# Kernel tuning notes

Hardware: AMD Instinct MI355X
Metric: run time of the kernel (lower is better)

## Reference

```python
import jax, jax.numpy as jnp
import numpy as np

HID = 256      # hidden_dim
EXPAND = 2
D_INNER = HID * EXPAND
LN_EPS = 1e-5


def _gru(xs, W_ih, W_hh, b_ih, b_hh):
    """torch nn.GRU (batch_first) over axis 1. xs: (N, P, d_inner) -> (N, P, H).
    Gate order (torch): r, z, n."""
    N = xs.shape[0]
    Hd = W_hh.shape[0]
    gi = xs @ W_ih + b_ih                 # (N, P, 3H) - input gates precomputed
    gi = jnp.swapaxes(gi, 0, 1)           # (P, N, 3H) for scan over P
    h0 = jnp.zeros((N, Hd), xs.dtype)

    def step(h, gi_t):
        gh = h @ W_hh + b_hh              # (N, 3H)
        ir, iz, i_n = jnp.split(gi_t, 3, axis=-1)
        hr, hz, h_n = jnp.split(gh, 3, axis=-1)
        r = jax.nn.sigmoid(ir + hr)
        z = jax.nn.sigmoid(iz + hz)
        n = jnp.tanh(i_n + r * h_n)
        h = (1.0 - z) * n + z * h
        return h, h

    _, ys = jax.lax.scan(step, h0, gi)    # (P, N, H)
    return jnp.swapaxes(ys, 0, 1)


def _branch(x2d, lin_W, lin_b, W_ih, W_hh, b_ih, b_hh):
    # Linear -> exact GELU (torch nn.GELU default) -> GRU
    h = jax.nn.gelu(x2d @ lin_W + lin_b, approximate=False)
    return _gru(h, W_ih, W_hh, b_ih, b_hh)


def setup_inputs() -> dict:
    key = jax.random.key(0)
    ks = jax.random.split(key, 16)
    s = 0.05
    p = {
        "x": jax.random.normal(ks[0], (8, 16, 1024, HID), jnp.float32),
        "fwd_lin_W": jax.random.normal(ks[1], (HID, D_INNER)) * s,
        "fwd_lin_b": jnp.zeros((D_INNER,)),
        "fwd_W_ih": jax.random.normal(ks[2], (D_INNER, 3 * HID)) * s,
        "fwd_W_hh": jax.random.normal(ks[3], (HID, 3 * HID)) * s,
        "fwd_b_ih": jnp.zeros((3 * HID,)),
        "fwd_b_hh": jnp.zeros((3 * HID,)),
        "bwd_lin_W": jax.random.normal(ks[4], (HID, D_INNER)) * s,
        "bwd_lin_b": jnp.zeros((D_INNER,)),
        "bwd_W_ih": jax.random.normal(ks[5], (D_INNER, 3 * HID)) * s,
        "bwd_W_hh": jax.random.normal(ks[6], (HID, 3 * HID)) * s,
        "bwd_b_ih": jnp.zeros((3 * HID,)),
        "bwd_b_hh": jnp.zeros((3 * HID,)),
        "proj_W": jax.random.normal(ks[7], (2 * HID, HID)) * s,
        "proj_b": jnp.zeros((HID,)),
        "ln_g": jnp.ones((HID,)),
        "ln_b": jnp.zeros((HID,)),
    }
    return p


def reference(x, fwd_lin_W, fwd_lin_b, fwd_W_ih, fwd_W_hh, fwd_b_ih, fwd_b_hh,
              bwd_lin_W, bwd_lin_b, bwd_W_ih, bwd_W_hh, bwd_b_ih, bwd_b_hh,
              proj_W, proj_b, ln_g, ln_b):
    B, T, P, H = x.shape
    xf = x.reshape(B * T, P, H)  # every timestep gets the identical spatial pass
    f_out = _branch(xf, fwd_lin_W, fwd_lin_b, fwd_W_ih, fwd_W_hh, fwd_b_ih, fwd_b_hh)
    b_out = _branch(xf[:, ::-1], bwd_lin_W, bwd_lin_b, bwd_W_ih, bwd_W_hh, bwd_b_ih, bwd_b_hh)[:, ::-1]
    cat = jnp.concatenate([f_out, b_out], axis=-1)          # (BT, P, 2H)
    out = cat @ proj_W + proj_b                              # (BT, P, H)
    out = out.reshape(B, T, P, H) + x                        # residual
    mu = out.mean(-1, keepdims=True)
    var = out.var(-1, keepdims=True)
    return (out - mu) * jax.lax.rsqrt(var + LN_EPS) * ln_g + ln_b
```

## Files before the change

kernel.cpp:

```cpp
#include <hip/hip_runtime.h>
#include <cmath>


typedef _Float16 h8  __attribute__((ext_vector_type(8)));
typedef _Float16 h2v __attribute__((ext_vector_type(2)));
typedef float    f32x4 __attribute__((ext_vector_type(4)));

#define MTOT 131072L
#define PSEQ 1024

__device__ __forceinline__ float fast_sigmoid(float x) {
    float e = __builtin_amdgcn_exp2f(-1.44269504089f * x);
    return __builtin_amdgcn_rcpf(1.f + e);
}
__device__ __forceinline__ float fast_tanh(float x) {
    float e = __builtin_amdgcn_exp2f(-2.88539008178f * x);
    return (1.f - e) * __builtin_amdgcn_rcpf(1.f + e);
}

template <int MODE>
__global__ __launch_bounds__(256) void k_gemm(
    const void* __restrict__ Aa_, const void* __restrict__ Ab_,
    const float* __restrict__ B, const float* __restrict__ bias,
    const float* __restrict__ xres, void* __restrict__ out_, long m_off)
{
    constexpr int K = (MODE == 0) ? 256 : 512;
    constexpr int N = (MODE == 0) ? 512 : (MODE == 1 ? 768 : 256);

    __shared__ __align__(16) _Float16 Al[64][40];
    __shared__ __align__(16) _Float16 Bl[64][40];

    const int tid  = threadIdx.x;
    const int lane = tid & 63;
    const int wave = tid >> 6;
    const int wm = wave >> 1, wn = wave & 1;
    const long bm0 = (long)(MODE == 1 ? blockIdx.y : blockIdx.x) * 64;
    const int  bn0 = (MODE == 1 ? blockIdx.x : blockIdx.y) * 64;

    const int sm  = tid >> 2;
    const int ska = (tid & 3) * 8;
    const int sn  = tid & 63;
    const int skb = (tid >> 6) * 8;

    f32x4 acc[2][2] = {};

    for (int kt = 0; kt < K / 32; ++kt) {
        h8 av;
        if constexpr (MODE == 0) {
            const float* ap = (const float*)Aa_ + (bm0 + sm) * 256 + kt * 32 + ska;
            #pragma unroll
            for (int i = 0; i < 8; ++i) av[i] = (_Float16)ap[i];
        } else if constexpr (MODE == 1) {
            av = *(const h8*)((const _Float16*)Aa_ + (bm0 + sm) * 512 + kt * 32 + ska);
        } else {
            const _Float16* src = (kt < 8) ? (const _Float16*)Aa_ : (const _Float16*)Ab_;
            av = *(const h8*)(src + (bm0 + sm) * 256 + (kt & 7) * 32 + ska);
        }
        *(h8*)&Al[sm][ska] = av;

        h8 bv;
        #pragma unroll
        for (int i = 0; i < 8; ++i)
            bv[i] = (_Float16)B[(long)(kt * 32 + skb + i) * N + bn0 + sn];
        *(h8*)&Bl[sn][skb] = bv;

        __syncthreads();

        const int fr = lane & 15, fg = lane >> 4;
        h8 a0 = *(const h8*)&Al[wm * 32 +      fr][fg * 8];
        h8 a1 = *(const h8*)&Al[wm * 32 + 16 + fr][fg * 8];
        h8 b0 = *(const h8*)&Bl[wn * 32 +      fr][fg * 8];
        h8 b1 = *(const h8*)&Bl[wn * 32 + 16 + fr][fg * 8];
        acc[0][0] = __builtin_amdgcn_mfma_f32_16x16x32_f16(a0, b0, acc[0][0], 0, 0, 0);
        acc[0][1] = __builtin_amdgcn_mfma_f32_16x16x32_f16(a0, b1, acc[0][1], 0, 0, 0);
        acc[1][0] = __builtin_amdgcn_mfma_f32_16x16x32_f16(a1, b0, acc[1][0], 0, 0, 0);
        acc[1][1] = __builtin_amdgcn_mfma_f32_16x16x32_f16(a1, b1, acc[1][1], 0, 0, 0);

        __syncthreads();
    }

    const int fr = lane & 15, fg = lane >> 4;
    #pragma unroll
    for (int fm = 0; fm < 2; ++fm)
    #pragma unroll
    for (int fn = 0; fn < 2; ++fn)
    #pragma unroll
    for (int r = 0; r < 4; ++r) {
        long row = bm0 + wm * 32 + fm * 16 + fg * 4 + r;
        int  col = bn0 + wn * 32 + fn * 16 + fr;
        float v = acc[fm][fn][r] + bias[col];
        if constexpr (MODE == 0) {
            v = 0.5f * v * (1.0f + erff(v * 0.70710678118654752f));
            ((_Float16*)out_)[row * (long)N + col] = (_Float16)v;
        } else if constexpr (MODE == 1) {
            long grow = row + m_off;
            int seq = (int)(grow >> 10), p = (int)(grow & 1023);
            int blk = seq >> 4, srow = seq & 15;
            int g = col >> 8, ci = col & 255;
            int wv = ci >> 5, tp = (ci >> 4) & 1;
            int ln = (ci & 15) | ((srow >> 2) << 4);
            int e = tp * 4 + (srow & 3);
            long oidx = (((long)(blk * 1024 + p) * 3 + g) * 512 + (wv * 64 + ln)) * 8 + e;
            ((_Float16*)out_)[oidx] = (_Float16)v;
        } else {
            v += xres[row * 256 + col];
            ((float*)out_)[row * 256 + col] = v;
        }
    }
}

__global__ __launch_bounds__(256) void k_prep_frag(
    const float* __restrict__ Whh, _Float16* __restrict__ Wp)
{
    const int t = blockIdx.x * 256 + threadIdx.x;
    const int l = t & 63, f = t >> 6;
    const int kt = f & 7;
    const int q  = f >> 3;
    const int tp = q & 1;
    const int q2 = q >> 1;
    const int g  = q2 % 3, w = q2 / 3;
    const int col = g * 256 + w * 32 + tp * 16 + (l & 15);
    const int k0  = kt * 32 + (l >> 4) * 8;
    h8 v;
    #pragma unroll
    for (int i = 0; i < 8; ++i)
        v[i] = (_Float16)Whh[(long)(k0 + i) * 768 + col];
    ((h8*)Wp)[t] = v;
}

__global__ __launch_bounds__(256) void k_prep_bias(
    const float* __restrict__ bih, const float* __restrict__ bhh, float* __restrict__ bc)
{
    const int c = blockIdx.x * 256 + threadIdx.x;
    bc[c] = bih[c] + (c < 512 ? bhh[c] : 0.f);
}

__global__ __launch_bounds__(512, 2) void k_gru2(
    const _Float16* __restrict__ gpf, const _Float16* __restrict__ gpb,
    const _Float16* __restrict__ Wpf, const _Float16* __restrict__ Wpb,
    const float* __restrict__ bhhf, const float* __restrict__ bhhb,
    _Float16* __restrict__ hof, _Float16* __restrict__ hob)
{
    const int b = blockIdx.x;
    const int dir = b & 1;
    const int blk = b >> 1;
    const int t = threadIdx.x;
    const int w = t >> 6, l = t & 63;
    const int lr = l & 15, lq = l >> 4;

    const _Float16* gp  = dir ? gpb : gpf;
    const _Float16* Wp  = dir ? Wpb : Wpf;
    const float*    bhh = dir ? bhhb : bhhf;
    _Float16*       hoo = dir ? hob : hof;

    __shared__ __align__(16) h8 wn_lds[8192];
    __shared__ __align__(16) _Float16 hbuf[2][16][264];

    h8 bfrz[2][2][8];
    {
        const h8* src = (const h8*)Wp + (long)w * 48 * 64 + l;
        #pragma unroll
        for (int g = 0; g < 2; ++g)
        #pragma unroll
        for (int tp = 0; tp < 2; ++tp)
        #pragma unroll
        for (int kt = 0; kt < 8; ++kt)
            bfrz[g][tp][kt] = src[((g * 2 + tp) * 8 + kt) * 64];
        #pragma unroll
        for (int tp = 0; tp < 2; ++tp)
        #pragma unroll
        for (int kt = 0; kt < 8; ++kt)
            wn_lds[((w * 2 + tp) * 8 + kt) * 64 + l] = src[((4 + tp) * 8 + kt) * 64];
    }
    const int col0 = w * 32 + lr;
    const float bn0 = bhh[512 + col0];
    const float bn1 = bhh[512 + col0 + 16];

    for (int i = t; i < 2 * 16 * 264; i += 512) ((_Float16*)hbuf)[i] = (_Float16)0.f;
    __syncthreads();

    const int d = dir ? -1 : 1;
    int p = dir ? (PSEQ - 1) : 0;
    int cur = 0;
    const long tbase = (long)t * 8;
    const long bbase = (long)blk * 1024;
    float hold[2][4] = {};

    h8 gv0 = *(const h8*)(gp + ((bbase + p) * 3 + 0) * 4096 + tbase);
    h8 gv1 = *(const h8*)(gp + ((bbase + p) * 3 + 1) * 4096 + tbase);
    h8 gv2 = *(const h8*)(gp + ((bbase + p) * 3 + 2) * 4096 + tbase);

    for (int step = 0; step < PSEQ; ++step) {
        int pn = p + d;
        pn = pn < 0 ? 0 : (pn > PSEQ - 1 ? PSEQ - 1 : pn);
        h8 nv0 = *(const h8*)(gp + ((bbase + pn) * 3 + 0) * 4096 + tbase);
        h8 nv1 = *(const h8*)(gp + ((bbase + pn) * 3 + 1) * 4096 + tbase);
        h8 nv2 = *(const h8*)(gp + ((bbase + pn) * 3 + 2) * 4096 + tbase);

        h8 af[8];
        #pragma unroll
        for (int kt = 0; kt < 8; ++kt)
            af[kt] = *(const h8*)&hbuf[cur][lr][kt * 32 + lq * 8];

        f32x4 accr[2] = {}, accz[2] = {};
        #pragma unroll
        for (int kt = 0; kt < 8; ++kt) {
            #pragma unroll
            for (int tp = 0; tp < 2; ++tp) {
                accr[tp] = __builtin_amdgcn_mfma_f32_16x16x32_f16(af[kt], bfrz[0][tp][kt], accr[tp], 0, 0, 0);
                accz[tp] = __builtin_amdgcn_mfma_f32_16x16x32_f16(af[kt], bfrz[1][tp][kt], accz[tp], 0, 0, 0);
            }
        }

        float rr[2][4], zz[2][4];
        #pragma unroll
        for (int tp = 0; tp < 2; ++tp)
        #pragma unroll
        for (int r = 0; r < 4; ++r) {
            const int e = tp * 4 + r;
            rr[tp][r] = fast_sigmoid(accr[tp][r] + (float)gv0[e]);
            zz[tp][r] = fast_sigmoid(accz[tp][r] + (float)gv1[e]);
        }

        f32x4 accn[2] = {};
        #pragma unroll
        for (int kt = 0; kt < 8; ++kt) {
            h8 bfn0 = wn_lds[((w * 2 + 0) * 8 + kt) * 64 + l];
            h8 bfn1 = wn_lds[((w * 2 + 1) * 8 + kt) * 64 + l];
            accn[0] = __builtin_amdgcn_mfma_f32_16x16x32_f16(af[kt], bfn0, accn[0], 0, 0, 0);
            accn[1] = __builtin_amdgcn_mfma_f32_16x16x32_f16(af[kt], bfn1, accn[1], 0, 0, 0);
        }

        #pragma unroll
        for (int tp = 0; tp < 2; ++tp) {
            const int col = col0 + tp * 16;
            const float bn = tp ? bn1 : bn0;
            #pragma unroll
            for (int r = 0; r < 4; ++r) {
                const int e = tp * 4 + r;
                float nh = accn[tp][r] + bn;
                float nn = fast_tanh((float)gv2[e] + rr[tp][r] * nh);
                float h  = fmaf(zz[tp][r], hold[tp][r] - nn, nn);
                hold[tp][r] = h;
                _Float16 hf = (_Float16)h;
                const int row = lq * 4 + r;
                hbuf[cur ^ 1][row][col] = hf;
                hoo[((long)(blk * 16 + row) * PSEQ + p) * 256 + col] = hf;
            }
        }
        __syncthreads();

        cur ^= 1; p += d;
        gv0 = nv0; gv1 = nv1; gv2 = nv2;
    }
}

__global__ __launch_bounds__(256) void k_ln(
    const float* __restrict__ pre, const float* __restrict__ g,
    const float* __restrict__ b, float* __restrict__ out)
{
    const long row = (long)blockIdx.x * 4 + (threadIdx.x >> 6);
    const int lane = threadIdx.x & 63;
    const float4 v = *(const float4*)&pre[row * 256 + lane * 4];
    float s  = v.x + v.y + v.z + v.w;
    float s2 = v.x * v.x + v.y * v.y + v.z * v.z + v.w * v.w;
    #pragma unroll
    for (int off = 32; off > 0; off >>= 1) {
        s  += __shfl_xor(s, off);
        s2 += __shfl_xor(s2, off);
    }
    const float mu  = s * (1.f / 256.f);
    const float var = s2 * (1.f / 256.f) - mu * mu;
    const float inv = rsqrtf(var + 1e-5f);
    const float4 gg = *(const float4*)&g[lane * 4];
    const float4 bb = *(const float4*)&b[lane * 4];
    float4 o;
    o.x = (v.x - mu) * inv * gg.x + bb.x;
    o.y = (v.y - mu) * inv * gg.y + bb.y;
    o.z = (v.z - mu) * inv * gg.z + bb.z;
    o.w = (v.w - mu) * inv * gg.w + bb.w;
    *(float4*)&out[row * 256 + lane * 4] = o;
}

extern "C" void kernel_launch(void* const* d_in, const int* in_sizes, int n_in,
                              void* d_out, int out_size, void* d_ws, size_t ws_size,
                              hipStream_t stream)
{
    const float* x       = (const float*)d_in[0];
    const float* f_lin_W = (const float*)d_in[1];
    const float* f_lin_b = (const float*)d_in[2];
    const float* f_W_ih  = (const float*)d_in[3];
    const float* f_W_hh  = (const float*)d_in[4];
    const float* f_b_ih  = (const float*)d_in[5];
    const float* f_b_hh  = (const float*)d_in[6];
    const float* b_lin_W = (const float*)d_in[7];
    const float* b_lin_b = (const float*)d_in[8];
    const float* b_W_ih  = (const float*)d_in[9];
    const float* b_W_hh  = (const float*)d_in[10];
    const float* b_b_ih  = (const float*)d_in[11];
    const float* b_b_hh  = (const float*)d_in[12];
    const float* proj_W  = (const float*)d_in[13];
    const float* proj_b  = (const float*)d_in[14];
    const float* ln_g    = (const float*)d_in[15];
    const float* ln_bb   = (const float*)d_in[16];

    char* ws = (char*)d_ws;

    const size_t BASE   = 1 << 20;
    const size_t GI_PER = (size_t)MTOT * 768 * 2;
    const size_t H1_OFF = BASE + 2 * GI_PER;
    const size_t H1_FULL = (size_t)MTOT * 512 * 2 * 2;
    int chunks = (ws_size >= H1_OFF + H1_FULL) ? 1
               : (ws_size >= H1_OFF + H1_FULL / 4) ? 4 : 8;
    const long MC = MTOT / chunks;

    _Float16* wpf = (_Float16*)ws;
    _Float16* wpb = (_Float16*)(ws + 393216);
    float*    bcf = (float*)(ws + 786432);
    float*    bcb = (float*)(ws + 786432 + 3072);
    _Float16* gif = (_Float16*)(ws + BASE);
    _Float16* gib = (_Float16*)(ws + BASE + GI_PER);
    float*    pre = (float*)(ws + BASE);
    _Float16* h1f = (_Float16*)(ws + H1_OFF);
    _Float16* h1b = h1f + MC * 512;

    _Float16* hof = (_Float16*)d_out;
    _Float16* hob = hof + MTOT * 256;

    k_prep_frag<<<96, 256, 0, stream>>>(f_W_hh, wpf);
    k_prep_frag<<<96, 256, 0, stream>>>(b_W_hh, wpb);
    k_prep_bias<<<3, 256, 0, stream>>>(f_b_ih, f_b_hh, bcf);
    k_prep_bias<<<3, 256, 0, stream>>>(b_b_ih, b_b_hh, bcb);

    for (int c = 0; c < chunks; ++c) {
        const long r0 = c * MC;
        k_gemm<0><<<dim3(MC / 64, 8),  256, 0, stream>>>(x + r0 * 256, nullptr, f_lin_W, f_lin_b, nullptr, h1f, 0L);
        k_gemm<0><<<dim3(MC / 64, 8),  256, 0, stream>>>(x + r0 * 256, nullptr, b_lin_W, b_lin_b, nullptr, h1b, 0L);
        k_gemm<1><<<dim3(12, MC / 64), 256, 0, stream>>>(h1f, nullptr, f_W_ih, bcf, nullptr, gif, r0);
        k_gemm<1><<<dim3(12, MC / 64), 256, 0, stream>>>(h1b, nullptr, b_W_ih, bcb, nullptr, gib, r0);
    }
    k_gru2<<<16, 512, 0, stream>>>(gif, gib, wpf, wpb, f_b_hh, b_b_hh, hof, hob);
    k_gemm<2><<<dim3(MTOT / 64, 4), 256, 0, stream>>>(hof, hob, proj_W, proj_b, x, pre, 0L);
    k_ln<<<MTOT / 4, 256, 0, stream>>>(pre, ln_g, ln_bb, (float*)d_out);
}
```

Baseline: 2.898 ms.

## Rewrite GEMMs with 128x128 tiles, pre-transposed fp16 weights and direct LDS loads

Replaces the 64x64-tile GEMM kernel with a 128x128-tile version that computes a 4x4 MFMA fragment grid per wave. Weights are transposed and converted to fp16 once in prep kernels, so the B tile can be loaded with contiguous global-to-LDS transfers instead of strided per-element fp32 loads. The forward and backward input linears are fused into one GEMM with N=1024 writing a concatenated activation buffer. The larger tiles raise register use and LDS footprint, and chunk sizing now adapts to the workspace size.

Result: faster. 2.528 ms (-12.8%).

```diff
diff --git a/kernel.cpp b/kernel.cpp
--- a/kernel.cpp
+++ b/kernel.cpp
@@ -3,7 +3,6 @@
 
 
 typedef _Float16 h8  __attribute__((ext_vector_type(8)));
-typedef _Float16 h2v __attribute__((ext_vector_type(2)));
 typedef float    f32x4 __attribute__((ext_vector_type(4)));
 
 #define MTOT 131072L
@@ -18,95 +17,135 @@
     return (1.f - e) * __builtin_amdgcn_rcpf(1.f + e);
 }
 
+__device__ __forceinline__ void gl_lds16(const void* g, void* lds_wave_base, int lane) {
+#if defined(__has_builtin) && __has_builtin(__builtin_amdgcn_global_load_lds)
+    __builtin_amdgcn_global_load_lds(
+        (const __attribute__((address_space(1))) void*)g,
+        (__attribute__((address_space(3))) void*)lds_wave_base, 16, 0, 0);
+#else
+    *((h8*)lds_wave_base + lane) = *(const h8*)g;
+#endif
+}
+
 template <int MODE>
-__global__ __launch_bounds__(256) void k_gemm(
+__global__ __launch_bounds__(256) void k_gemm2(
     const void* __restrict__ Aa_, const void* __restrict__ Ab_,
-    const float* __restrict__ B, const float* __restrict__ bias,
+    const _Float16* __restrict__ Bt, const float* __restrict__ bias,
     const float* __restrict__ xres, void* __restrict__ out_, long m_off)
 {
-    constexpr int K = (MODE == 0) ? 256 : 512;
-    constexpr int N = (MODE == 0) ? 512 : (MODE == 1 ? 768 : 256);
-
-    __shared__ __align__(16) _Float16 Al[64][40];
-    __shared__ __align__(16) _Float16 Bl[64][40];
-
-    const int tid  = threadIdx.x;
-    const int lane = tid & 63;
-    const int wave = tid >> 6;
-    const int wm = wave >> 1, wn = wave & 1;
-    const long bm0 = (long)(MODE == 1 ? blockIdx.y : blockIdx.x) * 64;
-    const int  bn0 = (MODE == 1 ? blockIdx.x : blockIdx.y) * 64;
-
-    const int sm  = tid >> 2;
-    const int ska = (tid & 3) * 8;
-    const int sn  = tid & 63;
-    const int skb = (tid >> 6) * 8;
-
-    f32x4 acc[2][2] = {};
-
-    for (int kt = 0; kt < K / 32; ++kt) {
-        h8 av;
+    constexpr int K   = (MODE == 0) ? 256 : 512;
+    constexpr int NKT = K / 32;
+
+    __shared__ __align__(16) _Float16 Al[128 * 32];
+    __shared__ __align__(16) _Float16 Bl[128 * 32];
+
+    const int t  = threadIdx.x;
+    const int wv = t >> 6, l = t & 63;
+    const int fr = l & 15, fg = l >> 4;
+    const int wm = wv >> 1, wn = wv & 1;
+    const long bm0 = (long)blockIdx.x * 128;
+    const int  bn0 = blockIdx.y * 128;
+    const int sr = t >> 2, sc = t & 3;
+
+    f32x4 acc[4][4] = {};
+
+    for (int kt = 0; kt < NKT; ++kt) {
+        #pragma unroll
+        for (int q = 0; q < 2; ++q) {
+            const int r = q * 64 + sr;
+            const _Float16* g = Bt + (long)(bn0 + r) * K + kt * 32 + sc * 8;
+            gl_lds16(g, (char*)Bl + q * 4096 + wv * 1024, l);
+        }
         if constexpr (MODE == 0) {
-            const float* ap = (const float*)Aa_ + (bm0 + sm) * 256 + kt * 32 + ska;
-            #pragma unroll
-            for (int i = 0; i < 8; ++i) av[i] = (_Float16)ap[i];
+            #pragma unroll
+            for (int q = 0; q < 2; ++q) {
+                const int r = q * 64 + sr;
+                const float* xs = (const float*)Aa_ + (bm0 + r) * 256 + kt * 32 + sc * 8;
+                float4 v0 = *(const float4*)xs;
+                float4 v1 = *(const float4*)(xs + 4);
+                h8 hv;
+                hv[0] = (_Float16)v0.x; hv[1] = (_Float16)v0.y;
+                hv[2] = (_Float16)v0.z; hv[3] = (_Float16)v0.w;
+                hv[4] = (_Float16)v1.x; hv[5] = (_Float16)v1.y;
+                hv[6] = (_Float16)v1.z; hv[7] = (_Float16)v1.w;
+                *(h8*)((char*)Al + r * 64 + sc * 16) = hv;
+            }
         } else if constexpr (MODE == 1) {
-            av = *(const h8*)((const _Float16*)Aa_ + (bm0 + sm) * 512 + kt * 32 + ska);
+            #pragma unroll
+            for (int q = 0; q < 2; ++q) {
+                const int r = q * 64 + sr;
+                const _Float16* g = (const _Float16*)Aa_ + (bm0 + r) * 1024 + kt * 32 + sc * 8;
+                gl_lds16(g, (char*)Al + q * 4096 + wv * 1024, l);
+            }
         } else {
             const _Float16* src = (kt < 8) ? (const _Float16*)Aa_ : (const _Float16*)Ab_;
-            av = *(const h8*)(src + (bm0 + sm) * 256 + (kt & 7) * 32 + ska);
-        }
-        *(h8*)&Al[sm][ska] = av;
-
-        h8 bv;
-        #pragma unroll
-        for (int i = 0; i < 8; ++i)
-            bv[i] = (_Float16)B[(long)(kt * 32 + skb + i) * N + bn0 + sn];
-        *(h8*)&Bl[sn][skb] = bv;
-
+            #pragma unroll
+            for (int q = 0; q < 2; ++q) {
+                const int r = q * 64 + sr;
+                const _Float16* g = src + (bm0 + r) * 256 + (kt & 7) * 32 + sc * 8;
+                gl_lds16(g, (char*)Al + q * 4096 + wv * 1024, l);
+            }
+        }
         __syncthreads();
 
-        const int fr = lane & 15, fg = lane >> 4;
-        h8 a0 = *(const h8*)&Al[wm * 32 +      fr][fg * 8];
-        h8 a1 = *(const h8*)&Al[wm * 32 + 16 + fr][fg * 8];
-        h8 b0 = *(const h8*)&Bl[wn * 32 +      fr][fg * 8];
-        h8 b1 = *(const h8*)&Bl[wn * 32 + 16 + fr][fg * 8];
-        acc[0][0] = __builtin_amdgcn_mfma_f32_16x16x32_f16(a0, b0, acc[0][0], 0, 0, 0);
-        acc[0][1] = __builtin_amdgcn_mfma_f32_16x16x32_f16(a0, b1, acc[0][1], 0, 0, 0);
-        acc[1][0] = __builtin_amdgcn_mfma_f32_16x16x32_f16(a1, b0, acc[1][0], 0, 0, 0);
-        acc[1][1] = __builtin_amdgcn_mfma_f32_16x16x32_f16(a1, b1, acc[1][1], 0, 0, 0);
-
+        h8 af[4], bf[4];
+        #pragma unroll
+        for (int fm = 0; fm < 4; ++fm)
+            af[fm] = *(const h8*)((const char*)Al + (wm * 64 + fm * 16 + fr) * 64 + fg * 16);
+        #pragma unroll
+        for (int fn = 0; fn < 4; ++fn)
+            bf[fn] = *(const h8*)((const char*)Bl + (wn * 64 + fn * 16 + fr) * 64 + fg * 16);
+        #pragma unroll
+        for (int fm = 0; fm < 4; ++fm)
+        #pragma unroll
+        for (int fn = 0; fn < 4; ++fn)
+            acc[fm][fn] = __builtin_amdgcn_mfma_f32_16x16x32_f16(af[fm], bf[fn], acc[fm][fn], 0, 0, 0);
         __syncthreads();
     }
 
-    const int fr = lane & 15, fg = lane >> 4;
-    #pragma unroll
-    for (int fm = 0; fm < 2; ++fm)
-    #pragma unroll
-    for (int fn = 0; fn < 2; ++fn)
+    #pragma unroll
+    for (int fm = 0; fm < 4; ++fm)
+    #pragma unroll
+    for (int fn = 0; fn < 4; ++fn)
     #pragma unroll
     for (int r = 0; r < 4; ++r) {
-        long row = bm0 + wm * 32 + fm * 16 + fg * 4 + r;
-        int  col = bn0 + wn * 32 + fn * 16 + fr;
+        long row = bm0 + wm * 64 + fm * 16 + fg * 4 + r;
+        int  col = bn0 + wn * 64 + fn * 16 + fr;
         float v = acc[fm][fn][r] + bias[col];
         if constexpr (MODE == 0) {
             v = 0.5f * v * (1.0f + erff(v * 0.70710678118654752f));
-            ((_Float16*)out_)[row * (long)N + col] = (_Float16)v;
+            ((_Float16*)out_)[row * 1024 + col] = (_Float16)v;
         } else if constexpr (MODE == 1) {
             long grow = row + m_off;
             int seq = (int)(grow >> 10), p = (int)(grow & 1023);
             int blk = seq >> 4, srow = seq & 15;
             int g = col >> 8, ci = col & 255;
-            int wv = ci >> 5, tp = (ci >> 4) & 1;
+            int wvx = ci >> 5, tp = (ci >> 4) & 1;
             int ln = (ci & 15) | ((srow >> 2) << 4);
             int e = tp * 4 + (srow & 3);
-            long oidx = (((long)(blk * 1024 + p) * 3 + g) * 512 + (wv * 64 + ln)) * 8 + e;
+            long oidx = (((long)(blk * 1024 + p) * 3 + g) * 512 + (wvx * 64 + ln)) * 8 + e;
             ((_Float16*)out_)[oidx] = (_Float16)v;
         } else {
             v += xres[row * 256 + col];
             ((float*)out_)[row * 256 + col] = v;
         }
     }
+}
+
+__global__ __launch_bounds__(256) void k_prep_wt(
+    const float* __restrict__ src, _Float16* __restrict__ dst, int Kd, int Nd)
+{
+    const int i = blockIdx.x * 256 + threadIdx.x;
+    if (i >= Kd * Nd) return;
+    const int n = i / Kd, k = i % Kd;
+    dst[i] = (_Float16)src[(long)k * Nd + n];
+}
+
+__global__ __launch_bounds__(256) void k_prep_lb(
+    const float* __restrict__ fb, const float* __restrict__ bb, float* __restrict__ dst)
+{
+    const int i = blockIdx.x * 256 + threadIdx.x;
+    dst[i] = (i < 512) ? fb[i] : bb[i - 512];
 }
 
 __global__ __launch_bounds__(256) void k_prep_frag(
@@ -306,40 +345,55 @@
 
     char* ws = (char*)d_ws;
 
-    const size_t BASE   = 1 << 20;
+    size_t o = 0;
+    _Float16* wt_lin  = (_Float16*)(ws + o); o += 1024 * 256 * 2;
+    _Float16* wt_ihf  = (_Float16*)(ws + o); o += 768 * 512 * 2;
+    _Float16* wt_ihb  = (_Float16*)(ws + o); o += 768 * 512 * 2;
+    _Float16* wt_proj = (_Float16*)(ws + o); o += 256 * 512 * 2;
+    float*    bl_lin  = (float*)(ws + o);    o += 1024 * 4;
+    float*    bcf     = (float*)(ws + o);    o += 768 * 4;
+    float*    bcb     = (float*)(ws + o);    o += 768 * 4;
+    _Float16* wpf     = (_Float16*)(ws + o); o += 393216;
+    _Float16* wpb     = (_Float16*)(ws + o); o += 393216;
+
+    const size_t BASE   = 4u << 20;
     const size_t GI_PER = (size_t)MTOT * 768 * 2;
-    const size_t H1_OFF = BASE + 2 * GI_PER;
-    const size_t H1_FULL = (size_t)MTOT * 512 * 2 * 2;
-    int chunks = (ws_size >= H1_OFF + H1_FULL) ? 1
-               : (ws_size >= H1_OFF + H1_FULL / 4) ? 4 : 8;
+    const size_t GI_END = BASE + 2 * GI_PER;
+    int chunks = 1;
+    while (GI_END + (size_t)(MTOT / chunks) * 1024 * 2 > ws_size && chunks < 16)
+        chunks <<= 1;
     const long MC = MTOT / chunks;
 
-    _Float16* wpf = (_Float16*)ws;
-    _Float16* wpb = (_Float16*)(ws + 393216);
-    float*    bcf = (float*)(ws + 786432);
-    float*    bcb = (float*)(ws + 786432 + 3072);
-    _Float16* gif = (_Float16*)(ws + BASE);
-    _Float16* gib = (_Float16*)(ws + BASE + GI_PER);
-    float*    pre = (float*)(ws + BASE);
-    _Float16* h1f = (_Float16*)(ws + H1_OFF);
-    _Float16* h1b = h1f + MC * 512;
+    _Float16* gif   = (_Float16*)(ws + BASE);
+    _Float16* gib   = (_Float16*)(ws + BASE + GI_PER);
+    float*    pre   = (float*)(ws + BASE);
+    _Float16* h1cat = (_Float16*)(ws + GI_END);
 
     _Float16* hof = (_Float16*)d_out;
     _Float16* hob = hof + MTOT * 256;
 
+    k_prep_wt<<<512,  256, 0, stream>>>(f_lin_W, wt_lin,             256, 512);
+    k_prep_wt<<<512,  256, 0, stream>>>(b_lin_W, wt_lin + 512 * 256, 256, 512);
+    k_prep_wt<<<1536, 256, 0, stream>>>(f_W_ih,  wt_ihf,             512, 768);
+    k_prep_wt<<<1536, 256, 0, stream>>>(b_W_ih,  wt_ihb,             512, 768);
+    k_prep_wt<<<512,  256, 0, stream>>>(proj_W,  wt_proj,            512, 256);
+    k_prep_lb<<<4,    256, 0, stream>>>(f_lin_b, b_lin_b, bl_lin);
+    k_prep_bias<<<3,  256, 0, stream>>>(f_b_ih, f_b_hh, bcf);
+    k_prep_bias<<<3,  256, 0, stream>>>(b_b_ih, b_b_hh, bcb);
     k_prep_frag<<<96, 256, 0, stream>>>(f_W_hh, wpf);
     k_prep_frag<<<96, 256, 0, stream>>>(b_W_hh, wpb);
-    k_prep_bias<<<3, 256, 0, stream>>>(f_b_ih, f_b_hh, bcf);
-    k_prep_bias<<<3, 256, 0, stream>>>(b_b_ih, b_b_hh, bcb);
 
     for (int c = 0; c < chunks; ++c) {
         const long r0 = c * MC;
-        k_gemm<0><<<dim3(MC / 64, 8),  256, 0, stream>>>(x + r0 * 256, nullptr, f_lin_W, f_lin_b, nullptr, h1f, 0L);
-        k_gemm<0><<<dim3(MC / 64, 8),  256, 0, stream>>>(x + r0 * 256, nullptr, b_lin_W, b_lin_b, nullptr, h1b, 0L);
-        k_gemm<1><<<dim3(12, MC / 64), 256, 0, stream>>>(h1f, nullptr, f_W_ih, bcf, nullptr, gif, r0);
-        k_gemm<1><<<dim3(12, MC / 64), 256, 0, stream>>>(h1b, nullptr, b_W_ih, bcb, nullptr, gib, r0);
+        k_gemm2<0><<<dim3(MC / 128, 8), 256, 0, stream>>>(
+            x + r0 * 256, nullptr, wt_lin, bl_lin, nullptr, h1cat, 0L);
+        k_gemm2<1><<<dim3(MC / 128, 6), 256, 0, stream>>>(
+            h1cat, nullptr, wt_ihf, bcf, nullptr, gif, r0);
+        k_gemm2<1><<<dim3(MC / 128, 6), 256, 0, stream>>>(
+            h1cat + 512, nullptr, wt_ihb, bcb, nullptr, gib, r0);
     }
     k_gru2<<<16, 512, 0, stream>>>(gif, gib, wpf, wpb, f_b_hh, b_b_hh, hof, hob);
-    k_gemm<2><<<dim3(MTOT / 64, 4), 256, 0, stream>>>(hof, hob, proj_W, proj_b, x, pre, 0L);
+    k_gemm2<2><<<dim3(MTOT / 128, 2), 256, 0, stream>>>(
+        hof, hob, wt_proj, proj_b, x, pre, 0L);
     k_ln<<<MTOT / 4, 256, 0, stream>>>(pre, ln_g, ln_bb, (float*)d_out);
 }
```
